# Kernel tuning notes

Hardware: AMD Instinct MI355X
Metric: run time of the kernel (lower is better)

Reference implementation:

```python
import jax, jax.numpy as jnp
from jax import lax
import numpy as np

D_MODEL = 6      # problemDim
ED = 48          # d_inner = expand_factor * d_model = hidden_size
N = 32           # d_state
DCONV = 16       # d_conv
NLAYERS = 2
DT_RANK = 1      # ceil(d_model / 16)
NCLS = 4
B, L = 16, 1024
EPS = 1e-5


def setup_inputs() -> dict:
    key = jax.random.key(0)
    ks = jax.random.split(key, 12)
    rn = lambda k, s, sc=0.1: (jax.random.normal(k, s, dtype=jnp.float32) * sc)
    return {
        "x": jax.random.normal(ks[0], (B, L, D_MODEL), dtype=jnp.float32),
        "in_proj_w": rn(ks[1], (NLAYERS, D_MODEL, 2 * ED)),
        "conv_w": rn(ks[2], (NLAYERS, ED, DCONV)),
        "conv_b": jnp.zeros((NLAYERS, ED), jnp.float32),
        "x_proj_w": rn(ks[3], (NLAYERS, ED, DT_RANK + 2 * N)),
        "dt_w": rn(ks[4], (NLAYERS, DT_RANK, ED), 1.0),
        "dt_b": rn(ks[5], (NLAYERS, ED), 0.5),
        # S4D-real init: A = -[1..N]
        "A_log": jnp.log(jnp.broadcast_to(jnp.arange(1, N + 1, dtype=jnp.float32), (NLAYERS, ED, N))),
        "D": jnp.ones((NLAYERS, ED), jnp.float32),
        "norm_w": jnp.ones((NLAYERS, D_MODEL), jnp.float32),
        "out_proj_w": rn(ks[6], (NLAYERS - 1, ED, D_MODEL)),
        "fc_w": rn(ks[7], (ED, ED)),
        "fc_b": jnp.zeros((ED,), jnp.float32),
        "cls_w": rn(ks[8], (ED, NCLS)),
        "cls_b": jnp.zeros((NCLS,), jnp.float32),
        "reg_w": rn(ks[9], (ED, 1)),
        "reg_b": jnp.zeros((1,), jnp.float32),
    }


def rmsnorm(h, w):
    return h * lax.rsqrt(jnp.mean(h * h, axis=-1, keepdims=True) + EPS) * w


def dwconv_causal(xs, w, b):
    # xs: (B,L,ED), w: (ED,DCONV), b: (ED,) -> causal depthwise conv, output length L
    u = jnp.pad(xs.transpose(0, 2, 1), ((0, 0), (0, 0), (DCONV - 1, 0)))  # (B,ED,L+DCONV-1)
    out = lax.conv_general_dilated(u, w[:, None, :], window_strides=(1,), padding="VALID",
                                   feature_group_count=ED,
                                   dimension_numbers=("NCH", "OIH", "NCH"))  # (B,ED,L)
    return (out + b[None, :, None]).transpose(0, 2, 1)


def selective_scan(deltaA, deltaBx, Cm):
    # deltaA, deltaBx: (B,L,ED,N); Cm: (B,L,N) -> y: (B,L,ED)
    dA = deltaA.transpose(1, 0, 2, 3)
    dBx = deltaBx.transpose(1, 0, 2, 3)
    Ct = Cm.transpose(1, 0, 2)

    def step(h, inp):
        dA_t, dBx_t, C_t = inp
        h = dA_t * h + dBx_t                       # (B,ED,N)
        y = jnp.einsum("ben,bn->be", h, C_t)       # (B,ED)
        return h, y

    h0 = jnp.zeros(dA.shape[1:], dA.dtype)
    _, ys = lax.scan(step, h0, (dA, dBx, Ct))
    return ys.transpose(1, 0, 2)


def mamba_forward(x, in_proj_w, conv_w, conv_b, x_proj_w, dt_w, dt_b, A_log, D,
                  norm_w, out_proj_w, fc_w, fc_b, cls_w, cls_b, reg_w, reg_b):
    h = x
    for i in range(NLAYERS):
        res = h
        u = rmsnorm(h, norm_w[i])
        xz = u @ in_proj_w[i]                      # (B,L,2*ED)
        xs, z = jnp.split(xz, 2, axis=-1)
        xs = jax.nn.silu(dwconv_causal(xs, conv_w[i], conv_b[i]))
        dbc = xs @ x_proj_w[i]                     # (B,L,DT_RANK+2N)
        dlt = dbc[..., :DT_RANK]
        Bm = dbc[..., DT_RANK:DT_RANK + N]
        Cm = dbc[..., DT_RANK + N:]
        delta = jax.nn.softplus(dlt @ dt_w[i] + dt_b[i])   # (B,L,ED)
        A = -jnp.exp(A_log[i])                     # (ED,N)
        deltaA = jnp.exp(delta[..., None] * A)     # (B,L,ED,N)
        deltaBx = delta[..., None] * Bm[:, :, None, :] * xs[..., None]
        y = selective_scan(deltaA, deltaBx, Cm) + D[i] * xs
        y = y * jax.nn.silu(z)
        if i < NLAYERS - 1:
            h = y @ out_proj_w[i] + res
        else:
            h = y  # classifer=True: last block exposes d_inner (=hidden_size) features
    feat = jax.nn.relu(h[:, -1, :] @ fc_w + fc_b)  # (B,ED)
    class_logits = feat @ cls_w + cls_b            # (B,NCLS)
    mass_pred = (feat @ reg_w + reg_b)[..., 0]     # (B,)
    return class_logits, mass_pred


def reference(x, in_proj_w, conv_w, conv_b, x_proj_w, dt_w, dt_b, A_log, D,
              norm_w, out_proj_w, fc_w, fc_b, cls_w, cls_b, reg_w, reg_b):
    return mamba_forward(x, in_proj_w, conv_w, conv_b, x_proj_w, dt_w, dt_b, A_log, D,
                         norm_w, out_proj_w, fc_w, fc_b, cls_w, cls_b, reg_w, reg_b)
```

## Files before the change

kernel.cpp:

```cpp
#include <hip/hip_runtime.h>
#include <math.h>

#define BB 16
#define LL 1024
#define DM 6
#define ED 48
#define NST 32
#define DCONVK 16
#define NCLS 4
#define CH 16
#define HALO 15
#define SNC 16
#define SCS 64

__device__ __forceinline__ float softplus_f(float x) {
    return fmaxf(x, 0.f) + log1pf(expf(-fabsf(x)));
}
__device__ __forceinline__ float silu_f(float x) {
    return x / (1.f + __expf(-x));
}

template<int MODE>
__global__ __launch_bounds__(256, 4) void pre_kernel(
    const float* __restrict__ hin,
    const float* __restrict__ ygT_in,
    const float* __restrict__ opw,
    const float* __restrict__ ipw,
    const float* __restrict__ nw,
    const float* __restrict__ cw,
    const float* __restrict__ cb,
    const float* __restrict__ xpw,
    const float* __restrict__ dtw,
    const float* __restrict__ dtb,
    float* __restrict__ xT,
    float* __restrict__ zT,
    float* __restrict__ dT,
    float* __restrict__ Bi,
    float* __restrict__ Ci)
{
    __shared__ float s_ipw[6*96];
    __shared__ float s_nw[6];
    __shared__ float s_cw[48*DCONVK];
    __shared__ float s_cb[48];
    __shared__ float s_xpw[48*65];
    __shared__ float s_dtw[48];
    __shared__ float s_dtb[48];
    __shared__ float s_opw[48*6];
    __shared__ float s_pp[(CH+HALO)*4*6];
    __shared__ float s_u[(CH+HALO)*7];
    __shared__ float s_raw[(CH+HALO)*49];
    __shared__ float s_xsT[48*CH];
    __shared__ float s_bc[64*(CH+1)];
    __shared__ float s_dlt[CH];

    const int tid = threadIdx.x;
    const int b  = blockIdx.x >> 6;
    const int l0 = (blockIdx.x & 63) * CH;
    const int ROWS = CH + HALO;

    for (int i = tid; i < 6*96; i += 256) s_ipw[i] = ipw[i];
    if (tid < 6) s_nw[tid] = nw[tid];
    for (int i = tid; i < 48*DCONVK; i += 256) s_cw[i] = cw[i];
    if (tid < 48) s_cb[tid] = cb[tid];
    for (int i = tid; i < 48*65; i += 256) s_xpw[i] = xpw[i];
    if (tid < 48) { s_dtw[tid] = dtw[tid]; s_dtb[tid] = dtb[tid]; }
    if (MODE == 1) for (int i = tid; i < 48*6; i += 256) s_opw[i] = opw[i];
    __syncthreads();

    if (MODE == 0) {
        if (tid < ROWS) {
            int l = l0 - HALO + tid;
            float u[DM];
            if (l >= 0) {
                float ss = 0.f;
                const float* hp = hin + ((size_t)b*LL + l)*DM;
                #pragma unroll
                for (int d = 0; d < DM; ++d) { u[d] = hp[d]; ss += u[d]*u[d]; }
                float sc = rsqrtf(ss * (1.f/DM) + 1e-5f);
                #pragma unroll
                for (int d = 0; d < DM; ++d) u[d] *= sc * s_nw[d];
            } else {
                #pragma unroll
                for (int d = 0; d < DM; ++d) u[d] = 0.f;
            }
            #pragma unroll
            for (int d = 0; d < DM; ++d) s_u[tid*7+d] = u[d];
        }
        __syncthreads();
    } else {
        const int g = tid >> 6, t = tid & 63;
        if (t < ROWS) {
            int l = l0 - HALO + t;
            float pacc[DM] = {0,0,0,0,0,0};
            if (l >= 0) {
                for (int e = g*12; e < g*12 + 12; ++e) {
                    float v = ygT_in[((size_t)b*48 + e)*LL + l];
                    #pragma unroll
                    for (int d = 0; d < DM; ++d) pacc[d] += v * s_opw[e*DM+d];
                }
            }
            #pragma unroll
            for (int d = 0; d < DM; ++d) s_pp[(t*4+g)*DM+d] = pacc[d];
        }
        __syncthreads();
        if (tid < ROWS) {
            int l = l0 - HALO + tid;
            float u[DM];
            if (l >= 0) {
                const float* xr = hin + ((size_t)b*LL + l)*DM;
                float ss = 0.f;
                #pragma unroll
                for (int d = 0; d < DM; ++d) {
                    float hv = s_pp[(tid*4+0)*DM+d] + s_pp[(tid*4+1)*DM+d]
                             + s_pp[(tid*4+2)*DM+d] + s_pp[(tid*4+3)*DM+d] + xr[d];
                    u[d] = hv; ss += hv*hv;
                }
                float sc = rsqrtf(ss * (1.f/DM) + 1e-5f);
                #pragma unroll
                for (int d = 0; d < DM; ++d) u[d] *= sc * s_nw[d];
            } else {
                #pragma unroll
                for (int d = 0; d < DM; ++d) u[d] = 0.f;
            }
            #pragma unroll
            for (int d = 0; d < DM; ++d) s_u[tid*7+d] = u[d];
        }
        __syncthreads();
    }

    for (int i = tid; i < 96*ROWS; i += 256) {
        int j = i / ROWS, t = i - j*ROWS;
        float acc = 0.f;
        #pragma unroll
        for (int d = 0; d < DM; ++d) acc += s_u[t*7+d]*s_ipw[d*96+j];
        if (j < 48) s_raw[t*49+j] = acc;
        else if (t >= HALO)
            zT[((size_t)b*48 + (j-48))*LL + (l0 - HALO + t)] = silu_f(acc);
    }
    __syncthreads();

    for (int o = tid; o < 48*CH; o += 256) {
        int c = o >> 4, p = o & 15;
        float acc = s_cb[c];
        #pragma unroll
        for (int k = 0; k < DCONVK; ++k)
            acc += s_raw[(p+k)*49 + c] * s_cw[c*DCONVK + k];
        float v = silu_f(acc);
        s_xsT[c*CH + p] = v;
        xT[((size_t)b*48 + c)*LL + l0 + p] = v;
    }
    __syncthreads();

    {
        const int j = tid >> 2, g = tid & 3;
        float a0=0,a1=0,a2=0,a3=0;
        for (int e = 0; e < 48; ++e) {
            float4 xv = *(const float4*)&s_xsT[e*CH + 4*g];
            float w = s_xpw[e*65 + 1 + j];
            a0 = fmaf(xv.x, w, a0); a1 = fmaf(xv.y, w, a1);
            a2 = fmaf(xv.z, w, a2); a3 = fmaf(xv.w, w, a3);
        }
        s_bc[j*(CH+1) + 4*g+0] = a0; s_bc[j*(CH+1) + 4*g+1] = a1;
        s_bc[j*(CH+1) + 4*g+2] = a2; s_bc[j*(CH+1) + 4*g+3] = a3;
    }
    if (tid < CH) {
        float acc = 0.f;
        for (int e = 0; e < 48; ++e) acc += s_xsT[e*CH + tid]*s_xpw[e*65];
        s_dlt[tid] = acc;
    }
    __syncthreads();

    for (int o = tid; o < 2*CH*32; o += 256) {
        int which = o >> 9;
        int l = (o >> 5) & (CH-1), n = o & 31;
        float v = s_bc[(which*32 + n)*(CH+1) + l];
        float* dst = which ? Ci : Bi;
        dst[((size_t)b*LL + l0 + l)*32 + n] = v;
    }

    for (int o = tid; o < 48*CH; o += 256) {
        int e = o >> 4, p = o & 15;
        float xv = s_dlt[p]*s_dtw[e] + s_dtb[e];
        dT[((size_t)b*48 + e)*LL + l0 + p] = softplus_f(xv);
    }
}

__global__ __launch_bounds__(512, 6) void scan_fused(
    const float* __restrict__ dT,
    const float* __restrict__ xT,
    const float* __restrict__ zT,
    const float* __restrict__ Bi,
    const float* __restrict__ Ci,
    const float* __restrict__ A_log,
    const float* __restrict__ Dw,
    float* __restrict__ ygT)
{
    __shared__ float2 sPH[SNC][32];
    __shared__ float2 sACa[SNC][32];
    __shared__ float  sYL[SNC][SCS];
    __shared__ float  sS [SNC][SCS];

    const int tid = threadIdx.x;
    const int lane = tid & 63;
    const int ch = lane >> 5, n = lane & 31;
    const int c = (tid >> 6)*2 + ch;
    const int b = blockIdx.x / 48;
    const int e = blockIdx.x % 48;

    const float Ac = -__expf(A_log[e*NST + n]);
    const float Dc = Dw[e];

    const size_t eb = ((size_t)b*48 + e)*LL + c*SCS;
    const float4* dp = (const float4*)(dT + eb);
    const float4* xp = (const float4*)(xT + eb);
    const float*  bp = Bi + ((size_t)b*LL + c*SCS)*32 + n;
    const float*  cp = Ci + ((size_t)b*LL + c*SCS)*32 + n;

    float h = 0.f, S = 0.f;

    #pragma unroll
    for (int q = 0; q < SCS/4; ++q) {
        float4 d4 = dp[q], x4 = xp[q];
        float b0 = bp[(4*q+0)*32], b1 = bp[(4*q+1)*32];
        float b2 = bp[(4*q+2)*32], b3 = bp[(4*q+3)*32];
        float c0 = cp[(4*q+0)*32], c1 = cp[(4*q+1)*32];
        float c2 = cp[(4*q+2)*32], c3 = cp[(4*q+3)*32];
        float p0, p1, p2, p3;
        h = fmaf(__expf(d4.x*Ac), h, d4.x*x4.x*b0); p0 = h*c0;
        h = fmaf(__expf(d4.y*Ac), h, d4.y*x4.y*b1); p1 = h*c1;
        h = fmaf(__expf(d4.z*Ac), h, d4.z*x4.z*b2); p2 = h*c2;
        h = fmaf(__expf(d4.w*Ac), h, d4.w*x4.w*b3); p3 = h*c3;
        float s0 = S + d4.x, s1 = s0 + d4.y, s2 = s1 + d4.z, s3 = s2 + d4.w;
        S = s3;
        if (n == 0) *(float4*)&sS[c][4*q] = make_float4(s0, s1, s2, s3);
        float q0 = p0 + __shfl_xor(p0, 16);
        float q1 = p1 + __shfl_xor(p1, 16);
        float q2 = p2 + __shfl_xor(p2, 16);
        float q3 = p3 + __shfl_xor(p3, 16);
        float m01 = (n & 16) ? q1 : q0;
        float m23 = (n & 16) ? q3 : q2;
        m01 += __shfl_xor(m01, 8);
        m23 += __shfl_xor(m23, 8);
        float mm = (n & 8) ? m23 : m01;
        mm += __shfl_xor(mm, 4);
        mm += __shfl_xor(mm, 2);
        mm += __shfl_xor(mm, 1);
        if ((n & 7) == 0) {
            int vidx = ((n >> 4) & 1) | (((n >> 3) & 1) << 1);
            float xv = (vidx & 2) ? ((vidx & 1) ? x4.w : x4.z)
                                  : ((vidx & 1) ? x4.y : x4.x);
            sYL[c][4*q + vidx] = fmaf(Dc, xv, mm);
        }
    }
    sPH[c][n] = make_float2(__expf(Ac*S), h);
    __syncthreads();

    if (tid < 32) {
        float2 v[SNC];
        #pragma unroll
        for (int k = 0; k < SNC; ++k) v[k] = sPH[k][tid];
        float acc = 0.f;
        #pragma unroll
        for (int k = 0; k < SNC; ++k) {
            sACa[k][tid] = make_float2(Ac, acc);
            acc = fmaf(v[k].x, acc, v[k].y);
        }
    }
    __syncthreads();

    #pragma unroll
    for (int r = 0; r < 2; ++r) {
        const int c2 = (tid >> 6) + 8*r;
        const int t = lane;
        const float St = sS[c2][t];
        const float yl = sYL[c2][t];
        const float4* cpt = (const float4*)(Ci + ((size_t)b*LL + c2*SCS + t)*32);
        float corr = 0.f;
        #pragma unroll
        for (int k = 0; k < 8; ++k) {
            float4 cv = cpt[k];
            float4 w0 = *(const float4*)&sACa[c2][4*k];
            float4 w1 = *(const float4*)&sACa[c2][4*k+2];
            corr = fmaf(cv.x * __expf(w0.x*St), w0.y, corr);
            corr = fmaf(cv.y * __expf(w0.z*St), w0.w, corr);
            corr = fmaf(cv.z * __expf(w1.x*St), w1.y, corr);
            corr = fmaf(cv.w * __expf(w1.z*St), w1.w, corr);
        }
        const size_t o = ((size_t)b*48 + e)*LL + c2*SCS + t;
        ygT[o] = (yl + corr) * zT[o];
    }
}

__global__ __launch_bounds__(1024) void head_kernel(
    const float* __restrict__ ygT,
    const float* __restrict__ fcw, const float* __restrict__ fcb,
    const float* __restrict__ clw, const float* __restrict__ clb,
    const float* __restrict__ rgw, const float* __restrict__ rgb,
    float* __restrict__ out)
{
    __shared__ float s_h[BB*48];
    __shared__ float s_f[BB*48];
    const int tid = threadIdx.x;
    const int b = tid >> 6, j = tid & 63;
    if (j < 48) s_h[b*48+j] = ygT[((size_t)b*48 + j)*LL + (LL-1)];
    __syncthreads();
    if (j < 48) {
        float acc = fcb[j];
        for (int k = 0; k < 48; ++k) acc += s_h[b*48+k]*fcw[k*48+j];
        s_f[b*48+j] = fmaxf(acc, 0.f);
    }
    __syncthreads();
    if (j < NCLS) {
        float acc = clb[j];
        for (int k = 0; k < 48; ++k) acc += s_f[b*48+k]*clw[k*NCLS+j];
        out[b*NCLS + j] = acc;
    }
    if (j == NCLS) {
        float acc = rgb[0];
        for (int k = 0; k < 48; ++k) acc += s_f[b*48+k]*rgw[k];
        out[BB*NCLS + b] = acc;
    }
}

extern "C" void kernel_launch(void* const* d_in, const int* in_sizes, int n_in,
                              void* d_out, int out_size, void* d_ws, size_t ws_size,
                              hipStream_t stream)
{
    const float* x     = (const float*)d_in[0];
    const float* ipw   = (const float*)d_in[1];
    const float* cw    = (const float*)d_in[2];
    const float* cb    = (const float*)d_in[3];
    const float* xpw   = (const float*)d_in[4];
    const float* dtw   = (const float*)d_in[5];
    const float* dtb   = (const float*)d_in[6];
    const float* A_log = (const float*)d_in[7];
    const float* Dw    = (const float*)d_in[8];
    const float* nw    = (const float*)d_in[9];
    const float* opw   = (const float*)d_in[10];
    const float* fcw   = (const float*)d_in[11];
    const float* fcb   = (const float*)d_in[12];
    const float* clw   = (const float*)d_in[13];
    const float* clb   = (const float*)d_in[14];
    const float* rgw   = (const float*)d_in[15];
    const float* rgb   = (const float*)d_in[16];
    float* out = (float*)d_out;

    float* ws = (float*)d_ws;
    const size_t BL = (size_t)BB*LL;
    float* xT  = ws;
    float* zT  = xT  + BL*48;
    float* dT  = zT  + BL*48;
    float* Bi  = dT  + BL*48;
    float* Ci  = Bi  + BL*32;
    float* ygT = Ci  + BL*32;

    const dim3 preGrid(BB*64), preBlk(256);
    const dim3 scanGrid(BB*48), scanBlk(512);

    pre_kernel<0><<<preGrid, preBlk, 0, stream>>>(
        x, nullptr, nullptr, ipw, nw, cw, cb, xpw, dtw, dtb,
        xT, zT, dT, Bi, Ci);
    scan_fused<<<scanGrid, scanBlk, 0, stream>>>(
        dT, xT, zT, Bi, Ci, A_log, Dw, ygT);

    pre_kernel<1><<<preGrid, preBlk, 0, stream>>>(
        x, ygT, opw, ipw + 6*96, nw + 6, cw + 48*DCONVK, cb + 48,
        xpw + 48*65, dtw + 48, dtb + 48,
        xT, zT, dT, Bi, Ci);
    scan_fused<<<scanGrid, scanBlk, 0, stream>>>(
        dT, xT, zT, Bi, Ci, A_log + 48*NST, Dw + 48, ygT);

    head_kernel<<<dim3(1), dim3(1024), 0, stream>>>(
        ygT, fcw, fcb, clw, clb, rgw, rgb, out);
}
```

Baseline: 194.4 us.

## Fuse all stages into a persistent megakernel with grid-wide atomic barriers

Replaces the five separate launches (two pre stages, two scan stages, head) with one persistent kernel of 256 blocks of 1024 threads. The stages are separated by software grid barriers built on an atomic counter, and a tiny init kernel resets the counter first. The pre stage now handles 64-position tiles instead of 16, which cuts the redundant conv-halo work, and each block runs 512-thread scan sub-units over two rounds. The aim is to remove launch gaps and inter-kernel drains. In exchange, occupancy during the scan is lower and half the threads do duplicate, discarded work in the second scan round. Correctness relies on all 256 blocks being co-resident, since otherwise the spin barrier deadlocks.

```diff
diff --git a/kernel.cpp b/kernel.cpp
--- a/kernel.cpp
+++ b/kernel.cpp
@@ -4,15 +4,32 @@
 #define BB 16
 #define LL 1024
 #define DM 6
-#define ED 48
 #define NST 32
 #define DCONVK 16
 #define NCLS 4
-#define CH 16
+
+#define NBLK 256
+#define BT   1024
+#define PCH  64
 #define HALO 15
+#define PROWS (PCH + HALO)
 #define SNC 16
 #define SCS 64
 
+#define O_U    0
+#define O_IPW  4160
+#define O_NW   4736
+#define O_CW   4744
+#define O_CB   5512
+#define O_XPW  5560
+#define O_DTW  8680
+#define O_DTB  8728
+#define O_OPW  8776
+#define O_SU   9064
+#define O_XST  9624
+#define O_DLT  12696
+#define SMEM_F 12768
+
 __device__ __forceinline__ float softplus_f(float x) {
     return fmaxf(x, 0.f) + log1pf(expf(-fabsf(x)));
 }
@@ -20,55 +37,52 @@
     return x / (1.f + __expf(-x));
 }
 
+__device__ __forceinline__ void gbar(unsigned* cnt, unsigned target) {
+    __syncthreads();
+    if (threadIdx.x == 0) {
+        __threadfence();
+        __hip_atomic_fetch_add(cnt, 1u, __ATOMIC_RELEASE, __HIP_MEMORY_SCOPE_AGENT);
+        for (int it = 0; it < 10000000; ++it) {
+            if (__hip_atomic_load(cnt, __ATOMIC_ACQUIRE, __HIP_MEMORY_SCOPE_AGENT) >= target)
+                break;
+            __builtin_amdgcn_s_sleep(2);
+        }
+        __threadfence();
+    }
+    __syncthreads();
+}
+
 template<int MODE>
-__global__ __launch_bounds__(256, 4) void pre_kernel(
-    const float* __restrict__ hin,
-    const float* __restrict__ ygT_in,
-    const float* __restrict__ opw,
-    const float* __restrict__ ipw,
-    const float* __restrict__ nw,
-    const float* __restrict__ cw,
-    const float* __restrict__ cb,
-    const float* __restrict__ xpw,
-    const float* __restrict__ dtw,
-    const float* __restrict__ dtb,
-    float* __restrict__ xT,
-    float* __restrict__ zT,
-    float* __restrict__ dT,
-    float* __restrict__ Bi,
-    float* __restrict__ Ci)
+__device__ void pre_block(
+    int b, int l0,
+    const float* __restrict__ hin, const float* __restrict__ ygT_in,
+    const float* __restrict__ opw, const float* __restrict__ ipw,
+    const float* __restrict__ nw,  const float* __restrict__ cw,
+    const float* __restrict__ cb,  const float* __restrict__ xpw,
+    const float* __restrict__ dtw, const float* __restrict__ dtb,
+    float* __restrict__ xT, float* __restrict__ zT, float* __restrict__ dT,
+    float* __restrict__ Bi, float* __restrict__ Ci, float* sm)
 {
-    __shared__ float s_ipw[6*96];
-    __shared__ float s_nw[6];
-    __shared__ float s_cw[48*DCONVK];
-    __shared__ float s_cb[48];
-    __shared__ float s_xpw[48*65];
-    __shared__ float s_dtw[48];
-    __shared__ float s_dtb[48];
-    __shared__ float s_opw[48*6];
-    __shared__ float s_pp[(CH+HALO)*4*6];
-    __shared__ float s_u[(CH+HALO)*7];
-    __shared__ float s_raw[(CH+HALO)*49];
-    __shared__ float s_xsT[48*CH];
-    __shared__ float s_bc[64*(CH+1)];
-    __shared__ float s_dlt[CH];
-
     const int tid = threadIdx.x;
-    const int b  = blockIdx.x >> 6;
-    const int l0 = (blockIdx.x & 63) * CH;
-    const int ROWS = CH + HALO;
-
-    for (int i = tid; i < 6*96; i += 256) s_ipw[i] = ipw[i];
+    float* s_ipw = sm + O_IPW;  float* s_nw  = sm + O_NW;
+    float* s_cw  = sm + O_CW;   float* s_cb  = sm + O_CB;
+    float* s_xpw = sm + O_XPW;  float* s_dtw = sm + O_DTW;
+    float* s_dtb = sm + O_DTB;  float* s_opw = sm + O_OPW;
+    float* s_u   = sm + O_SU;   float* s_xsT = sm + O_XST;
+    float* s_dlt = sm + O_DLT;
+    float* s_pp  = sm + O_U;    float* s_raw = sm + O_U;  float* s_bc = sm + O_U;
+
+    for (int i = tid; i < 576; i += BT) s_ipw[i] = ipw[i];
     if (tid < 6) s_nw[tid] = nw[tid];
-    for (int i = tid; i < 48*DCONVK; i += 256) s_cw[i] = cw[i];
+    for (int i = tid; i < 768; i += BT) s_cw[i] = cw[i];
     if (tid < 48) s_cb[tid] = cb[tid];
-    for (int i = tid; i < 48*65; i += 256) s_xpw[i] = xpw[i];
+    for (int i = tid; i < 3120; i += BT) s_xpw[i] = xpw[i];
     if (tid < 48) { s_dtw[tid] = dtw[tid]; s_dtb[tid] = dtb[tid]; }
-    if (MODE == 1) for (int i = tid; i < 48*6; i += 256) s_opw[i] = opw[i];
+    if (MODE == 1) for (int i = tid; i < 288; i += BT) s_opw[i] = opw[i];
     __syncthreads();
 
     if (MODE == 0) {
-        if (tid < ROWS) {
+        if (tid < PROWS) {
             int l = l0 - HALO + tid;
             float u[DM];
             if (l >= 0) {
@@ -88,22 +102,22 @@
         }
         __syncthreads();
     } else {
-        const int g = tid >> 6, t = tid & 63;
-        if (t < ROWS) {
+        const int g = tid >> 7, t = tid & 127;
+        if (t < PROWS) {
             int l = l0 - HALO + t;
             float pacc[DM] = {0,0,0,0,0,0};
             if (l >= 0) {
-                for (int e = g*12; e < g*12 + 12; ++e) {
+                for (int e = g*6; e < g*6 + 6; ++e) {
                     float v = ygT_in[((size_t)b*48 + e)*LL + l];
                     #pragma unroll
                     for (int d = 0; d < DM; ++d) pacc[d] += v * s_opw[e*DM+d];
                 }
             }
             #pragma unroll
-            for (int d = 0; d < DM; ++d) s_pp[(t*4+g)*DM+d] = pacc[d];
-        }
-        __syncthreads();
-        if (tid < ROWS) {
+            for (int d = 0; d < DM; ++d) s_pp[(t*8+g)*DM+d] = pacc[d];
+        }
+        __syncthreads();
+        if (tid < PROWS) {
             int l = l0 - HALO + tid;
             float u[DM];
             if (l >= 0) {
@@ -111,8 +125,9 @@
                 float ss = 0.f;
                 #pragma unroll
                 for (int d = 0; d < DM; ++d) {
-                    float hv = s_pp[(tid*4+0)*DM+d] + s_pp[(tid*4+1)*DM+d]
-                             + s_pp[(tid*4+2)*DM+d] + s_pp[(tid*4+3)*DM+d] + xr[d];
+                    float hv = xr[d];
+                    #pragma unroll
+                    for (int g2 = 0; g2 < 8; ++g2) hv += s_pp[(tid*8+g2)*DM+d];
                     u[d] = hv; ss += hv*hv;
                 }
                 float sc = rsqrtf(ss * (1.f/DM) + 1e-5f);
@@ -128,8 +143,8 @@
         __syncthreads();
     }
 
-    for (int i = tid; i < 96*ROWS; i += 256) {
-        int j = i / ROWS, t = i - j*ROWS;
+    for (int i = tid; i < 96*PROWS; i += BT) {
+        int j = i / PROWS, t = i - j*PROWS;
         float acc = 0.f;
         #pragma unroll
         for (int d = 0; d < DM; ++d) acc += s_u[t*7+d]*s_ipw[d*96+j];
@@ -139,73 +154,75 @@
     }
     __syncthreads();
 
-    for (int o = tid; o < 48*CH; o += 256) {
-        int c = o >> 4, p = o & 15;
+    for (int o = tid; o < 48*PCH; o += BT) {
+        int c = o >> 6, p = o & 63;
         float acc = s_cb[c];
         #pragma unroll
         for (int k = 0; k < DCONVK; ++k)
             acc += s_raw[(p+k)*49 + c] * s_cw[c*DCONVK + k];
         float v = silu_f(acc);
-        s_xsT[c*CH + p] = v;
+        s_xsT[c*PCH + p] = v;
         xT[((size_t)b*48 + c)*LL + l0 + p] = v;
     }
     __syncthreads();
 
     {
-        const int j = tid >> 2, g = tid & 3;
+        const int j = tid >> 4, g = tid & 15;
         float a0=0,a1=0,a2=0,a3=0;
         for (int e = 0; e < 48; ++e) {
-            float4 xv = *(const float4*)&s_xsT[e*CH + 4*g];
+            float4 xv = *(const float4*)&s_xsT[e*PCH + 4*g];
             float w = s_xpw[e*65 + 1 + j];
             a0 = fmaf(xv.x, w, a0); a1 = fmaf(xv.y, w, a1);
             a2 = fmaf(xv.z, w, a2); a3 = fmaf(xv.w, w, a3);
         }
-        s_bc[j*(CH+1) + 4*g+0] = a0; s_bc[j*(CH+1) + 4*g+1] = a1;
-        s_bc[j*(CH+1) + 4*g+2] = a2; s_bc[j*(CH+1) + 4*g+3] = a3;
-    }
-    if (tid < CH) {
-        float acc = 0.f;
-        for (int e = 0; e < 48; ++e) acc += s_xsT[e*CH + tid]*s_xpw[e*65];
-        s_dlt[tid] = acc;
-    }
-    __syncthreads();
-
-    for (int o = tid; o < 2*CH*32; o += 256) {
-        int which = o >> 9;
-        int l = (o >> 5) & (CH-1), n = o & 31;
-        float v = s_bc[(which*32 + n)*(CH+1) + l];
+        s_bc[j*65 + 4*g+0] = a0; s_bc[j*65 + 4*g+1] = a1;
+        s_bc[j*65 + 4*g+2] = a2; s_bc[j*65 + 4*g+3] = a3;
+    }
+    if (tid < 16) {
+        float a0=0,a1=0,a2=0,a3=0;
+        for (int e = 0; e < 48; ++e) {
+            float4 xv = *(const float4*)&s_xsT[e*PCH + 4*tid];
+            float w = s_xpw[e*65];
+            a0 = fmaf(xv.x, w, a0); a1 = fmaf(xv.y, w, a1);
+            a2 = fmaf(xv.z, w, a2); a3 = fmaf(xv.w, w, a3);
+        }
+        s_dlt[4*tid+0] = a0; s_dlt[4*tid+1] = a1;
+        s_dlt[4*tid+2] = a2; s_dlt[4*tid+3] = a3;
+    }
+    __syncthreads();
+
+    for (int o = tid; o < 2*PCH*32; o += BT) {
+        int which = o >> 11;
+        int l = (o >> 5) & 63, n = o & 31;
+        float v = s_bc[(which*32 + n)*65 + l];
         float* dst = which ? Ci : Bi;
         dst[((size_t)b*LL + l0 + l)*32 + n] = v;
     }
 
-    for (int o = tid; o < 48*CH; o += 256) {
-        int e = o >> 4, p = o & 15;
+    for (int o = tid; o < 48*PCH; o += BT) {
+        int e = o >> 6, p = o & 63;
         float xv = s_dlt[p]*s_dtw[e] + s_dtb[e];
         dT[((size_t)b*48 + e)*LL + l0 + p] = softplus_f(xv);
     }
 }
 
-__global__ __launch_bounds__(512, 6) void scan_fused(
-    const float* __restrict__ dT,
-    const float* __restrict__ xT,
-    const float* __restrict__ zT,
-    const float* __restrict__ Bi,
-    const float* __restrict__ Ci,
-    const float* __restrict__ A_log,
-    const float* __restrict__ Dw,
-    float* __restrict__ ygT)
+__device__ void scan_unit(
+    int u, int wr, int sub,
+    const float* __restrict__ dT, const float* __restrict__ xT,
+    const float* __restrict__ zT, const float* __restrict__ Bi,
+    const float* __restrict__ Ci, const float* __restrict__ A_log,
+    const float* __restrict__ Dw, float* __restrict__ ygT, float* sm)
 {
-    __shared__ float2 sPH[SNC][32];
-    __shared__ float2 sACa[SNC][32];
-    __shared__ float  sYL[SNC][SCS];
-    __shared__ float  sS [SNC][SCS];
-
-    const int tid = threadIdx.x;
-    const int lane = tid & 63;
+    const int tid = threadIdx.x & 511;
+    const int lane = threadIdx.x & 63;
     const int ch = lane >> 5, n = lane & 31;
-    const int c = (tid >> 6)*2 + ch;
-    const int b = blockIdx.x / 48;
-    const int e = blockIdx.x % 48;
+    const int c = ((tid >> 6) << 1) | ch;
+    const int b = u / 48, e = u % 48;
+
+    float2* sPH  = (float2*)(sm + sub*4096);
+    float2* sACa = (float2*)(sm + sub*4096 + 1024);
+    float*  sYL  = sm + sub*4096 + 2048;
+    float*  sS   = sm + sub*4096 + 3072;
 
     const float Ac = -__expf(A_log[e*NST + n]);
     const float Dc = Dw[e];
@@ -232,7 +249,7 @@
         h = fmaf(__expf(d4.w*Ac), h, d4.w*x4.w*b3); p3 = h*c3;
         float s0 = S + d4.x, s1 = s0 + d4.y, s2 = s1 + d4.z, s3 = s2 + d4.w;
         S = s3;
-        if (n == 0) *(float4*)&sS[c][4*q] = make_float4(s0, s1, s2, s3);
+        if (n == 0) *(float4*)&sS[c*SCS + 4*q] = make_float4(s0, s1, s2, s3);
         float q0 = p0 + __shfl_xor(p0, 16);
         float q1 = p1 + __shfl_xor(p1, 16);
         float q2 = p2 + __shfl_xor(p2, 16);
@@ -249,20 +266,20 @@
             int vidx = ((n >> 4) & 1) | (((n >> 3) & 1) << 1);
             float xv = (vidx & 2) ? ((vidx & 1) ? x4.w : x4.z)
                                   : ((vidx & 1) ? x4.y : x4.x);
-            sYL[c][4*q + vidx] = fmaf(Dc, xv, mm);
-        }
-    }
-    sPH[c][n] = make_float2(__expf(Ac*S), h);
+            sYL[c*SCS + 4*q + vidx] = fmaf(Dc, xv, mm);
+        }
+    }
+    sPH[c*32 + n] = make_float2(__expf(Ac*S), h);
     __syncthreads();
 
     if (tid < 32) {
         float2 v[SNC];
         #pragma unroll
-        for (int k = 0; k < SNC; ++k) v[k] = sPH[k][tid];
+        for (int k = 0; k < SNC; ++k) v[k] = sPH[k*32 + tid];
         float acc = 0.f;
         #pragma unroll
         for (int k = 0; k < SNC; ++k) {
-            sACa[k][tid] = make_float2(Ac, acc);
+            sACa[k*32 + tid] = make_float2(Ac, acc);
             acc = fmaf(v[k].x, acc, v[k].y);
         }
     }
@@ -272,53 +289,95 @@
     for (int r = 0; r < 2; ++r) {
         const int c2 = (tid >> 6) + 8*r;
         const int t = lane;
-        const float St = sS[c2][t];
-        const float yl = sYL[c2][t];
+        const float St = sS[c2*SCS + t];
+        const float yl = sYL[c2*SCS + t];
         const float4* cpt = (const float4*)(Ci + ((size_t)b*LL + c2*SCS + t)*32);
         float corr = 0.f;
         #pragma unroll
         for (int k = 0; k < 8; ++k) {
             float4 cv = cpt[k];
-            float4 w0 = *(const float4*)&sACa[c2][4*k];
-            float4 w1 = *(const float4*)&sACa[c2][4*k+2];
+            float4 w0 = *(const float4*)&sACa[c2*32 + 4*k];
+            float4 w1 = *(const float4*)&sACa[c2*32 + 4*k + 2];
             corr = fmaf(cv.x * __expf(w0.x*St), w0.y, corr);
             corr = fmaf(cv.y * __expf(w0.z*St), w0.w, corr);
             corr = fmaf(cv.z * __expf(w1.x*St), w1.y, corr);
             corr = fmaf(cv.w * __expf(w1.z*St), w1.w, corr);
         }
-        const size_t o = ((size_t)b*48 + e)*LL + c2*SCS + t;
-        ygT[o] = (yl + corr) * zT[o];
-    }
-}
-
-__global__ __launch_bounds__(1024) void head_kernel(
-    const float* __restrict__ ygT,
-    const float* __restrict__ fcw, const float* __restrict__ fcb,
-    const float* __restrict__ clw, const float* __restrict__ clb,
-    const float* __restrict__ rgw, const float* __restrict__ rgb,
-    float* __restrict__ out)
+        if (wr) {
+            const size_t o = ((size_t)b*48 + e)*LL + c2*SCS + t;
+            ygT[o] = (yl + corr) * zT[o];
+        }
+    }
+}
+
+__global__ void init_kernel(unsigned* cnt) {
+    if (threadIdx.x == 0) *cnt = 0u;
+}
+
+__global__ __launch_bounds__(BT, 4) void mega_kernel(
+    const float* __restrict__ x,   const float* __restrict__ ipw,
+    const float* __restrict__ cw,  const float* __restrict__ cb,
+    const float* __restrict__ xpw, const float* __restrict__ dtw,
+    const float* __restrict__ dtb, const float* __restrict__ A_log,
+    const float* __restrict__ Dw,  const float* __restrict__ nw,
+    const float* __restrict__ opw, const float* __restrict__ fcw,
+    const float* __restrict__ fcb, const float* __restrict__ clw,
+    const float* __restrict__ clb, const float* __restrict__ rgw,
+    const float* __restrict__ rgb,
+    float* __restrict__ xT, float* __restrict__ zT, float* __restrict__ dT,
+    float* __restrict__ Bi, float* __restrict__ Ci, float* __restrict__ ygT,
+    float* __restrict__ out, unsigned* cnt)
 {
-    __shared__ float s_h[BB*48];
-    __shared__ float s_f[BB*48];
+    __shared__ float sm[SMEM_F];
+    const int blk = blockIdx.x;
     const int tid = threadIdx.x;
-    const int b = tid >> 6, j = tid & 63;
-    if (j < 48) s_h[b*48+j] = ygT[((size_t)b*48 + j)*LL + (LL-1)];
-    __syncthreads();
-    if (j < 48) {
-        float acc = fcb[j];
-        for (int k = 0; k < 48; ++k) acc += s_h[b*48+k]*fcw[k*48+j];
-        s_f[b*48+j] = fmaxf(acc, 0.f);
-    }
-    __syncthreads();
-    if (j < NCLS) {
-        float acc = clb[j];
-        for (int k = 0; k < 48; ++k) acc += s_f[b*48+k]*clw[k*NCLS+j];
-        out[b*NCLS + j] = acc;
-    }
-    if (j == NCLS) {
-        float acc = rgb[0];
-        for (int k = 0; k < 48; ++k) acc += s_f[b*48+k]*rgw[k];
-        out[BB*NCLS + b] = acc;
+    const int b_pre = blk >> 4, l0 = (blk & 15) * PCH;
+    const int sub = tid >> 9;
+
+    pre_block<0>(b_pre, l0, x, nullptr, nullptr, ipw, nw, cw, cb, xpw, dtw, dtb,
+                 xT, zT, dT, Bi, Ci, sm);
+    gbar(cnt, 1*NBLK);
+    for (int r = 0; r < 2; ++r) {
+        int u  = (r == 0) ? (blk*3 + sub) : (blk*3 + 2);
+        int wr = (r == 0) ? 1 : (sub == 0);
+        scan_unit(u, wr, sub, dT, xT, zT, Bi, Ci, A_log, Dw, ygT, sm);
+        __syncthreads();
+    }
+    gbar(cnt, 2*NBLK);
+
+    pre_block<1>(b_pre, l0, x, ygT, opw, ipw + 576, nw + 6, cw + 768, cb + 48,
+                 xpw + 3120, dtw + 48, dtb + 48, xT, zT, dT, Bi, Ci, sm);
+    gbar(cnt, 3*NBLK);
+    for (int r = 0; r < 2; ++r) {
+        int u  = (r == 0) ? (blk*3 + sub) : (blk*3 + 2);
+        int wr = (r == 0) ? 1 : (sub == 0);
+        scan_unit(u, wr, sub, dT, xT, zT, Bi, Ci, A_log + 1536, Dw + 48, ygT, sm);
+        __syncthreads();
+    }
+    gbar(cnt, 4*NBLK);
+
+    if (blk == 0) {
+        float* s_h = sm;
+        float* s_f = sm + 800;
+        const int b = tid >> 6, j = tid & 63;
+        if (j < 48) s_h[b*48+j] = ygT[((size_t)b*48 + j)*LL + (LL-1)];
+        __syncthreads();
+        if (j < 48) {
+            float acc = fcb[j];
+            for (int k = 0; k < 48; ++k) acc += s_h[b*48+k]*fcw[k*48+j];
+            s_f[b*48+j] = fmaxf(acc, 0.f);
+        }
+        __syncthreads();
+        if (j < NCLS) {
+            float acc = clb[j];
+            for (int k = 0; k < 48; ++k) acc += s_f[b*48+k]*clw[k*NCLS+j];
+            out[b*NCLS + j] = acc;
+        }
+        if (j == NCLS) {
+            float acc = rgb[0];
+            for (int k = 0; k < 48; ++k) acc += s_f[b*48+k]*rgw[k];
+            out[BB*NCLS + b] = acc;
+        }
     }
 }
 
@@ -353,23 +412,11 @@
     float* Bi  = dT  + BL*48;
     float* Ci  = Bi  + BL*32;
     float* ygT = Ci  + BL*32;
-
-    const dim3 preGrid(BB*64), preBlk(256);
-    const dim3 scanGrid(BB*48), scanBlk(512);
-
-    pre_kernel<0><<<preGrid, preBlk, 0, stream>>>(
-        x, nullptr, nullptr, ipw, nw, cw, cb, xpw, dtw, dtb,
-        xT, zT, dT, Bi, Ci);
-    scan_fused<<<scanGrid, scanBlk, 0, stream>>>(
-        dT, xT, zT, Bi, Ci, A_log, Dw, ygT);
-
-    pre_kernel<1><<<preGrid, preBlk, 0, stream>>>(
-        x, ygT, opw, ipw + 6*96, nw + 6, cw + 48*DCONVK, cb + 48,
-        xpw + 48*65, dtw + 48, dtb + 48,
-        xT, zT, dT, Bi, Ci);
-    scan_fused<<<scanGrid, scanBlk, 0, stream>>>(
-        dT, xT, zT, Bi, Ci, A_log + 48*NST, Dw + 48, ygT);
-
-    head_kernel<<<dim3(1), dim3(1024), 0, stream>>>(
-        ygT, fcw, fcb, clw, clb, rgw, rgb, out);
-}
+    unsigned* cnt = (unsigned*)(ws + (size_t)8*1024*1024);
+
+    init_kernel<<<dim3(1), dim3(64), 0, stream>>>(cnt);
+    mega_kernel<<<dim3(NBLK), dim3(BT), 0, stream>>>(
+        x, ipw, cw, cb, xpw, dtw, dtb, A_log, Dw, nw, opw,
+        fcw, fcb, clw, clb, rgw, rgb,
+        xT, zT, dT, Bi, Ci, ygT, out, cnt);
+}
```

Result: slower. 320.5 us (+64.9%).

## Restructure pre kernel to one-thread-per-timestep and add transposed C buffer

Applied to the files above, without the earlier changes.

The pre kernel is rewritten so each 64-thread block handles 64 timesteps and each thread computes a full timestep (conv, x_proj for B/C, delta) in registers, reading weights directly from global memory instead of staging them in shared memory. This cuts the halo recomputation ratio and most block-level syncs. C is also written in a transposed [b][n][l] layout so the scan's correction pass reads it coalesced across lanes. In exchange the grid shrinks to 256 small blocks with heavy per-thread register use and serial loops, and an extra C buffer is written.

```diff
diff --git a/kernel.cpp b/kernel.cpp
--- a/kernel.cpp
+++ b/kernel.cpp
@@ -4,12 +4,12 @@
 #define BB 16
 #define LL 1024
 #define DM 6
-#define ED 48
 #define NST 32
 #define DCONVK 16
 #define NCLS 4
-#define CH 16
+#define PCH 64
 #define HALO 15
+#define PROWS (PCH + HALO)
 #define SNC 16
 #define SCS 64
 
@@ -21,8 +21,8 @@
 }
 
 template<int MODE>
-__global__ __launch_bounds__(256, 4) void pre_kernel(
-    const float* __restrict__ hin,
+__global__ __launch_bounds__(64) void pre_kernel(
+    const float* __restrict__ xin,
     const float* __restrict__ ygT_in,
     const float* __restrict__ opw,
     const float* __restrict__ ipw,
@@ -36,152 +36,106 @@
     float* __restrict__ zT,
     float* __restrict__ dT,
     float* __restrict__ Bi,
-    float* __restrict__ Ci)
+    float* __restrict__ Ci,
+    float* __restrict__ CT)
 {
-    __shared__ float s_ipw[6*96];
-    __shared__ float s_nw[6];
-    __shared__ float s_cw[48*DCONVK];
-    __shared__ float s_cb[48];
-    __shared__ float s_xpw[48*65];
-    __shared__ float s_dtw[48];
-    __shared__ float s_dtb[48];
-    __shared__ float s_opw[48*6];
-    __shared__ float s_pp[(CH+HALO)*4*6];
-    __shared__ float s_u[(CH+HALO)*7];
-    __shared__ float s_raw[(CH+HALO)*49];
-    __shared__ float s_xsT[48*CH];
-    __shared__ float s_bc[64*(CH+1)];
-    __shared__ float s_dlt[CH];
+    __shared__ float s_raw[PROWS*49];
 
     const int tid = threadIdx.x;
-    const int b  = blockIdx.x >> 6;
-    const int l0 = (blockIdx.x & 63) * CH;
-    const int ROWS = CH + HALO;
-
-    for (int i = tid; i < 6*96; i += 256) s_ipw[i] = ipw[i];
-    if (tid < 6) s_nw[tid] = nw[tid];
-    for (int i = tid; i < 48*DCONVK; i += 256) s_cw[i] = cw[i];
-    if (tid < 48) s_cb[tid] = cb[tid];
-    for (int i = tid; i < 48*65; i += 256) s_xpw[i] = xpw[i];
-    if (tid < 48) { s_dtw[tid] = dtw[tid]; s_dtb[tid] = dtb[tid]; }
-    if (MODE == 1) for (int i = tid; i < 48*6; i += 256) s_opw[i] = opw[i];
-    __syncthreads();
-
-    if (MODE == 0) {
-        if (tid < ROWS) {
-            int l = l0 - HALO + tid;
-            float u[DM];
-            if (l >= 0) {
-                float ss = 0.f;
-                const float* hp = hin + ((size_t)b*LL + l)*DM;
-                #pragma unroll
-                for (int d = 0; d < DM; ++d) { u[d] = hp[d]; ss += u[d]*u[d]; }
-                float sc = rsqrtf(ss * (1.f/DM) + 1e-5f);
-                #pragma unroll
-                for (int d = 0; d < DM; ++d) u[d] *= sc * s_nw[d];
-            } else {
-                #pragma unroll
-                for (int d = 0; d < DM; ++d) u[d] = 0.f;
-            }
-            #pragma unroll
-            for (int d = 0; d < DM; ++d) s_u[tid*7+d] = u[d];
-        }
-        __syncthreads();
-    } else {
-        const int g = tid >> 6, t = tid & 63;
-        if (t < ROWS) {
-            int l = l0 - HALO + t;
-            float pacc[DM] = {0,0,0,0,0,0};
-            if (l >= 0) {
-                for (int e = g*12; e < g*12 + 12; ++e) {
+    const int b  = blockIdx.x >> 4;
+    const int l0 = (blockIdx.x & 15) * PCH;
+
+    for (int r = tid; r < PROWS; r += 64) {
+        const int l = l0 - HALO + r;
+        float u[DM] = {0,0,0,0,0,0};
+        if (l >= 0) {
+            const float* xr = xin + ((size_t)b*LL + l)*DM;
+            #pragma unroll
+            for (int d = 0; d < DM; ++d) u[d] = xr[d];
+            if (MODE == 1) {
+                for (int e = 0; e < 48; ++e) {
                     float v = ygT_in[((size_t)b*48 + e)*LL + l];
                     #pragma unroll
-                    for (int d = 0; d < DM; ++d) pacc[d] += v * s_opw[e*DM+d];
+                    for (int d = 0; d < DM; ++d) u[d] = fmaf(v, opw[e*DM+d], u[d]);
                 }
             }
-            #pragma unroll
-            for (int d = 0; d < DM; ++d) s_pp[(t*4+g)*DM+d] = pacc[d];
-        }
-        __syncthreads();
-        if (tid < ROWS) {
-            int l = l0 - HALO + tid;
-            float u[DM];
-            if (l >= 0) {
-                const float* xr = hin + ((size_t)b*LL + l)*DM;
-                float ss = 0.f;
+            float ss = 0.f;
+            #pragma unroll
+            for (int d = 0; d < DM; ++d) ss += u[d]*u[d];
+            float sc = rsqrtf(ss * (1.f/DM) + 1e-5f);
+            #pragma unroll
+            for (int d = 0; d < DM; ++d) u[d] *= sc * nw[d];
+        }
+        for (int j = 0; j < 48; ++j) {
+            float acc = 0.f;
+            #pragma unroll
+            for (int d = 0; d < DM; ++d) acc = fmaf(u[d], ipw[d*96+j], acc);
+            s_raw[r*49+j] = acc;
+        }
+        if (l >= l0) {
+            for (int j = 48; j < 96; ++j) {
+                float acc = 0.f;
                 #pragma unroll
-                for (int d = 0; d < DM; ++d) {
-                    float hv = s_pp[(tid*4+0)*DM+d] + s_pp[(tid*4+1)*DM+d]
-                             + s_pp[(tid*4+2)*DM+d] + s_pp[(tid*4+3)*DM+d] + xr[d];
-                    u[d] = hv; ss += hv*hv;
-                }
-                float sc = rsqrtf(ss * (1.f/DM) + 1e-5f);
-                #pragma unroll
-                for (int d = 0; d < DM; ++d) u[d] *= sc * s_nw[d];
-            } else {
-                #pragma unroll
-                for (int d = 0; d < DM; ++d) u[d] = 0.f;
+                for (int d = 0; d < DM; ++d) acc = fmaf(u[d], ipw[d*96+j], acc);
+                zT[((size_t)b*48 + (j-48))*LL + l] = silu_f(acc);
             }
-            #pragma unroll
-            for (int d = 0; d < DM; ++d) s_u[tid*7+d] = u[d];
-        }
-        __syncthreads();
-    }
-
-    for (int i = tid; i < 96*ROWS; i += 256) {
-        int j = i / ROWS, t = i - j*ROWS;
-        float acc = 0.f;
-        #pragma unroll
-        for (int d = 0; d < DM; ++d) acc += s_u[t*7+d]*s_ipw[d*96+j];
-        if (j < 48) s_raw[t*49+j] = acc;
-        else if (t >= HALO)
-            zT[((size_t)b*48 + (j-48))*LL + (l0 - HALO + t)] = silu_f(acc);
-    }
-    __syncthreads();
-
-    for (int o = tid; o < 48*CH; o += 256) {
-        int c = o >> 4, p = o & 15;
-        float acc = s_cb[c];
+        }
+    }
+    __syncthreads();
+
+    const int p = tid;
+    const int l = l0 + p;
+    float xs[48];
+    for (int c = 0; c < 48; ++c) {
+        float acc = cb[c];
         #pragma unroll
         for (int k = 0; k < DCONVK; ++k)
-            acc += s_raw[(p+k)*49 + c] * s_cw[c*DCONVK + k];
+            acc = fmaf(s_raw[(p+k)*49 + c], cw[c*DCONVK + k], acc);
         float v = silu_f(acc);
-        s_xsT[c*CH + p] = v;
-        xT[((size_t)b*48 + c)*LL + l0 + p] = v;
-    }
-    __syncthreads();
+        xs[c] = v;
+        xT[((size_t)b*48 + c)*LL + l] = v;
+    }
 
     {
-        const int j = tid >> 2, g = tid & 3;
-        float a0=0,a1=0,a2=0,a3=0;
+        float acc[32];
+        #pragma unroll
+        for (int n = 0; n < 32; ++n) acc[n] = 0.f;
         for (int e = 0; e < 48; ++e) {
-            float4 xv = *(const float4*)&s_xsT[e*CH + 4*g];
-            float w = s_xpw[e*65 + 1 + j];
-            a0 = fmaf(xv.x, w, a0); a1 = fmaf(xv.y, w, a1);
-            a2 = fmaf(xv.z, w, a2); a3 = fmaf(xv.w, w, a3);
-        }
-        s_bc[j*(CH+1) + 4*g+0] = a0; s_bc[j*(CH+1) + 4*g+1] = a1;
-        s_bc[j*(CH+1) + 4*g+2] = a2; s_bc[j*(CH+1) + 4*g+3] = a3;
-    }
-    if (tid < CH) {
-        float acc = 0.f;
-        for (int e = 0; e < 48; ++e) acc += s_xsT[e*CH + tid]*s_xpw[e*65];
-        s_dlt[tid] = acc;
-    }
-    __syncthreads();
-
-    for (int o = tid; o < 2*CH*32; o += 256) {
-        int which = o >> 9;
-        int l = (o >> 5) & (CH-1), n = o & 31;
-        float v = s_bc[(which*32 + n)*(CH+1) + l];
-        float* dst = which ? Ci : Bi;
-        dst[((size_t)b*LL + l0 + l)*32 + n] = v;
-    }
-
-    for (int o = tid; o < 48*CH; o += 256) {
-        int e = o >> 4, p = o & 15;
-        float xv = s_dlt[p]*s_dtw[e] + s_dtb[e];
-        dT[((size_t)b*48 + e)*LL + l0 + p] = softplus_f(xv);
+            const float xv = xs[e];
+            const float* w = xpw + e*65 + 1;
+            #pragma unroll
+            for (int n = 0; n < 32; ++n) acc[n] = fmaf(xv, w[n], acc[n]);
+        }
+        float4* bo = (float4*)(Bi + ((size_t)b*LL + l)*32);
+        #pragma unroll
+        for (int k = 0; k < 8; ++k)
+            bo[k] = make_float4(acc[4*k], acc[4*k+1], acc[4*k+2], acc[4*k+3]);
+    }
+    {
+        float acc[32];
+        #pragma unroll
+        for (int n = 0; n < 32; ++n) acc[n] = 0.f;
+        for (int e = 0; e < 48; ++e) {
+            const float xv = xs[e];
+            const float* w = xpw + e*65 + 33;
+            #pragma unroll
+            for (int n = 0; n < 32; ++n) acc[n] = fmaf(xv, w[n], acc[n]);
+        }
+        float4* co = (float4*)(Ci + ((size_t)b*LL + l)*32);
+        #pragma unroll
+        for (int k = 0; k < 8; ++k)
+            co[k] = make_float4(acc[4*k], acc[4*k+1], acc[4*k+2], acc[4*k+3]);
+        #pragma unroll
+        for (int n = 0; n < 32; ++n)
+            CT[((size_t)b*32 + n)*LL + l] = acc[n];
+    }
+    {
+        float dlt = 0.f;
+        for (int e = 0; e < 48; ++e) dlt = fmaf(xs[e], xpw[e*65], dlt);
+        for (int e = 0; e < 48; ++e) {
+            float xv = fmaf(dlt, dtw[e], dtb[e]);
+            dT[((size_t)b*48 + e)*LL + l] = softplus_f(xv);
+        }
     }
 }
 
@@ -191,6 +145,7 @@
     const float* __restrict__ zT,
     const float* __restrict__ Bi,
     const float* __restrict__ Ci,
+    const float* __restrict__ CT,
     const float* __restrict__ A_log,
     const float* __restrict__ Dw,
     float* __restrict__ ygT)
@@ -274,17 +229,12 @@
         const int t = lane;
         const float St = sS[c2][t];
         const float yl = sYL[c2][t];
-        const float4* cpt = (const float4*)(Ci + ((size_t)b*LL + c2*SCS + t)*32);
+        const float* ctp = CT + (size_t)b*32*LL + c2*SCS + t;
         float corr = 0.f;
         #pragma unroll
-        for (int k = 0; k < 8; ++k) {
-            float4 cv = cpt[k];
-            float4 w0 = *(const float4*)&sACa[c2][4*k];
-            float4 w1 = *(const float4*)&sACa[c2][4*k+2];
-            corr = fmaf(cv.x * __expf(w0.x*St), w0.y, corr);
-            corr = fmaf(cv.y * __expf(w0.z*St), w0.w, corr);
-            corr = fmaf(cv.z * __expf(w1.x*St), w1.y, corr);
-            corr = fmaf(cv.w * __expf(w1.z*St), w1.w, corr);
+        for (int n2 = 0; n2 < 32; ++n2) {
+            float2 w = sACa[c2][n2];
+            corr = fmaf(ctp[(size_t)n2*LL] * __expf(w.x*St), w.y, corr);
         }
         const size_t o = ((size_t)b*48 + e)*LL + c2*SCS + t;
         ygT[o] = (yl + corr) * zT[o];
@@ -352,23 +302,24 @@
     float* dT  = zT  + BL*48;
     float* Bi  = dT  + BL*48;
     float* Ci  = Bi  + BL*32;
-    float* ygT = Ci  + BL*32;
-
-    const dim3 preGrid(BB*64), preBlk(256);
+    float* CT  = Ci  + BL*32;
+    float* ygT = CT  + BL*32;
+
+    const dim3 preGrid(BB*16), preBlk(64);
     const dim3 scanGrid(BB*48), scanBlk(512);
 
     pre_kernel<0><<<preGrid, preBlk, 0, stream>>>(
         x, nullptr, nullptr, ipw, nw, cw, cb, xpw, dtw, dtb,
-        xT, zT, dT, Bi, Ci);
+        xT, zT, dT, Bi, Ci, CT);
     scan_fused<<<scanGrid, scanBlk, 0, stream>>>(
-        dT, xT, zT, Bi, Ci, A_log, Dw, ygT);
+        dT, xT, zT, Bi, Ci, CT, A_log, Dw, ygT);
 
     pre_kernel<1><<<preGrid, preBlk, 0, stream>>>(
-        x, ygT, opw, ipw + 6*96, nw + 6, cw + 48*DCONVK, cb + 48,
-        xpw + 48*65, dtw + 48, dtb + 48,
-        xT, zT, dT, Bi, Ci);
+        x, ygT, opw, ipw + 576, nw + 6, cw + 768, cb + 48,
+        xpw + 3120, dtw + 48, dtb + 48,
+        xT, zT, dT, Bi, Ci, CT);
     scan_fused<<<scanGrid, scanBlk, 0, stream>>>(
-        dT, xT, zT, Bi, Ci, A_log + 48*NST, Dw + 48, ygT);
+        dT, xT, zT, Bi, Ci, CT, A_log + 1536, Dw + 48, ygT);
 
     head_kernel<<<dim3(1), dim3(1024), 0, stream>>>(
         ygT, fcw, fcb, clw, clb, rgw, rgb, out);
```

Result: slower. 309.0 us (+59.0%).

## Split scan into 32 chunks of 32 with 1024-thread blocks and transposed C

Applied to the files above, without the earlier changes.

Doubles the number of scan chunks per (batch, channel) block to 32 chunks of 32 steps, running 1024 threads per block so each thread handles one output position in the correction pass. The pre kernel now also writes a transposed copy of C laid out (b, n, l) so the correction loop reads coalesced across t. The intent is a shorter serial chunk scan and more parallelism per block. The costs are a longer 32-step cross-chunk carry, an extra 2 MB of C writes, and larger blocks that may lower occupancy.

```diff
diff --git a/kernel.cpp b/kernel.cpp
--- a/kernel.cpp
+++ b/kernel.cpp
@@ -4,14 +4,13 @@
 #define BB 16
 #define LL 1024
 #define DM 6
-#define ED 48
 #define NST 32
 #define DCONVK 16
 #define NCLS 4
 #define CH 16
 #define HALO 15
-#define SNC 16
-#define SCS 64
+#define SNC 32
+#define SCS 32
 
 __device__ __forceinline__ float softplus_f(float x) {
     return fmaxf(x, 0.f) + log1pf(expf(-fabsf(x)));
@@ -36,7 +35,8 @@
     float* __restrict__ zT,
     float* __restrict__ dT,
     float* __restrict__ Bi,
-    float* __restrict__ Ci)
+    float* __restrict__ Ci,
+    float* __restrict__ CT)
 {
     __shared__ float s_ipw[6*96];
     __shared__ float s_nw[6];
@@ -177,6 +177,10 @@
         float* dst = which ? Ci : Bi;
         dst[((size_t)b*LL + l0 + l)*32 + n] = v;
     }
+    for (int o = tid; o < 32*CH; o += 256) {
+        int n = o >> 4, l = o & (CH-1);
+        CT[((size_t)b*32 + n)*LL + l0 + l] = s_bc[(32+n)*(CH+1) + l];
+    }
 
     for (int o = tid; o < 48*CH; o += 256) {
         int e = o >> 4, p = o & 15;
@@ -185,12 +189,13 @@
     }
 }
 
-__global__ __launch_bounds__(512, 6) void scan_fused(
+__global__ __launch_bounds__(1024, 8) void scan_fused(
     const float* __restrict__ dT,
     const float* __restrict__ xT,
     const float* __restrict__ zT,
     const float* __restrict__ Bi,
     const float* __restrict__ Ci,
+    const float* __restrict__ CT,
     const float* __restrict__ A_log,
     const float* __restrict__ Dw,
     float* __restrict__ ygT)
@@ -203,7 +208,7 @@
     const int tid = threadIdx.x;
     const int lane = tid & 63;
     const int ch = lane >> 5, n = lane & 31;
-    const int c = (tid >> 6)*2 + ch;
+    const int c = ((tid >> 6) << 1) | ch;
     const int b = blockIdx.x / 48;
     const int e = blockIdx.x % 48;
 
@@ -256,35 +261,32 @@
     __syncthreads();
 
     if (tid < 32) {
-        float2 v[SNC];
-        #pragma unroll
-        for (int k = 0; k < SNC; ++k) v[k] = sPH[k][tid];
         float acc = 0.f;
         #pragma unroll
-        for (int k = 0; k < SNC; ++k) {
-            sACa[k][tid] = make_float2(Ac, acc);
-            acc = fmaf(v[k].x, acc, v[k].y);
-        }
-    }
-    __syncthreads();
-
-    #pragma unroll
-    for (int r = 0; r < 2; ++r) {
-        const int c2 = (tid >> 6) + 8*r;
-        const int t = lane;
+        for (int batch = 0; batch < 4; ++batch) {
+            float2 v[8];
+            #pragma unroll
+            for (int k = 0; k < 8; ++k) v[k] = sPH[batch*8+k][tid];
+            #pragma unroll
+            for (int k = 0; k < 8; ++k) {
+                sACa[batch*8+k][tid] = make_float2(Ac, acc);
+                acc = fmaf(v[k].x, acc, v[k].y);
+            }
+        }
+    }
+    __syncthreads();
+
+    {
+        const int c2 = tid >> 5;
+        const int t = tid & 31;
         const float St = sS[c2][t];
         const float yl = sYL[c2][t];
-        const float4* cpt = (const float4*)(Ci + ((size_t)b*LL + c2*SCS + t)*32);
+        const float* ctp = CT + (size_t)b*32*LL + c2*SCS + t;
         float corr = 0.f;
         #pragma unroll
-        for (int k = 0; k < 8; ++k) {
-            float4 cv = cpt[k];
-            float4 w0 = *(const float4*)&sACa[c2][4*k];
-            float4 w1 = *(const float4*)&sACa[c2][4*k+2];
-            corr = fmaf(cv.x * __expf(w0.x*St), w0.y, corr);
-            corr = fmaf(cv.y * __expf(w0.z*St), w0.w, corr);
-            corr = fmaf(cv.z * __expf(w1.x*St), w1.y, corr);
-            corr = fmaf(cv.w * __expf(w1.z*St), w1.w, corr);
+        for (int n2 = 0; n2 < 32; ++n2) {
+            float2 w = sACa[c2][n2];
+            corr = fmaf(ctp[(size_t)n2*LL] * __expf(w.x*St), w.y, corr);
         }
         const size_t o = ((size_t)b*48 + e)*LL + c2*SCS + t;
         ygT[o] = (yl + corr) * zT[o];
@@ -352,23 +354,24 @@
     float* dT  = zT  + BL*48;
     float* Bi  = dT  + BL*48;
     float* Ci  = Bi  + BL*32;
-    float* ygT = Ci  + BL*32;
+    float* CT  = Ci  + BL*32;
+    float* ygT = CT  + BL*32;
 
     const dim3 preGrid(BB*64), preBlk(256);
-    const dim3 scanGrid(BB*48), scanBlk(512);
+    const dim3 scanGrid(BB*48), scanBlk(1024);
 
     pre_kernel<0><<<preGrid, preBlk, 0, stream>>>(
         x, nullptr, nullptr, ipw, nw, cw, cb, xpw, dtw, dtb,
-        xT, zT, dT, Bi, Ci);
+        xT, zT, dT, Bi, Ci, CT);
     scan_fused<<<scanGrid, scanBlk, 0, stream>>>(
-        dT, xT, zT, Bi, Ci, A_log, Dw, ygT);
+        dT, xT, zT, Bi, Ci, CT, A_log, Dw, ygT);
 
     pre_kernel<1><<<preGrid, preBlk, 0, stream>>>(
-        x, ygT, opw, ipw + 6*96, nw + 6, cw + 48*DCONVK, cb + 48,
-        xpw + 48*65, dtw + 48, dtb + 48,
-        xT, zT, dT, Bi, Ci);
+        x, ygT, opw, ipw + 576, nw + 6, cw + 768, cb + 48,
+        xpw + 3120, dtw + 48, dtb + 48,
+        xT, zT, dT, Bi, Ci, CT);
     scan_fused<<<scanGrid, scanBlk, 0, stream>>>(
-        dT, xT, zT, Bi, Ci, A_log + 48*NST, Dw + 48, ygT);
+        dT, xT, zT, Bi, Ci, CT, A_log + 1536, Dw + 48, ygT);
 
     head_kernel<<<dim3(1), dim3(1024), 0, stream>>>(
         ygT, fcw, fcb, clw, clb, rgw, rgb, out);
```

Result: faster. 179.7 us (-7.6%).
